# Performance work log

Hardware: AMD Instinct MI355X
Metric: run time of the kernel (lower is better)

The kernel has to match this reference:

```python
import jax, jax.numpy as jnp
import numpy as np

N_NODES = 10000
N_EDGES = 320000
IN_DIM = 512
HID = 64
H0 = 8
OUT = 64
H1 = 1
NEG_SLOPE = 0.2


def gat_layer(h, src, dst, W, attn_l, attn_r, n_nodes, activation=None):
    # h: (N, F_in); W: (F_in, H*D); attn_l/attn_r: (H, D)
    H, D = attn_l.shape
    feat = (h @ W).reshape(n_nodes, H, D)            # (N, H, D)
    el = jnp.einsum('nhd,hd->nh', feat, attn_l)      # (N, H)
    er = jnp.einsum('nhd,hd->nh', feat, attn_r)      # (N, H)
    e = jax.nn.leaky_relu(el[src] + er[dst], NEG_SLOPE)  # (E, H)
    # edge softmax over incoming edges of each destination node
    m = jax.ops.segment_max(e, dst, num_segments=n_nodes)   # (N, H), -inf for isolated
    m = jnp.where(jnp.isfinite(m), m, 0.0)
    ex = jnp.exp(e - m[dst])                         # (E, H)
    s = jax.ops.segment_sum(ex, dst, num_segments=n_nodes)  # (N, H)
    alpha = ex / s[dst]                              # (E, H)
    # weighted aggregation: out[dst] += alpha * feat[src]
    out = jax.ops.segment_sum(alpha[:, :, None] * feat[src], dst,
                              num_segments=n_nodes)  # (N, H, D)
    if activation is not None:
        out = activation(out)
    return out


def setup_inputs() -> dict:
    key = jax.random.key(0)
    ks = jax.random.split(key, 9)
    h = jax.random.normal(ks[0], (N_NODES, IN_DIM), dtype=jnp.float32)
    src = jax.random.randint(ks[1], (N_EDGES,), 0, N_NODES, dtype=jnp.int32)
    dst = jax.random.randint(ks[2], (N_EDGES,), 0, N_NODES, dtype=jnp.int32)
    W1 = jax.random.normal(ks[3], (IN_DIM, H0 * HID), dtype=jnp.float32) / np.sqrt(IN_DIM)
    attn_l1 = jax.random.normal(ks[4], (H0, HID), dtype=jnp.float32) / np.sqrt(HID)
    attn_r1 = jax.random.normal(ks[5], (H0, HID), dtype=jnp.float32) / np.sqrt(HID)
    W2 = jax.random.normal(ks[6], (H0 * HID, H1 * OUT), dtype=jnp.float32) / np.sqrt(H0 * HID)
    attn_l2 = jax.random.normal(ks[7], (H1, OUT), dtype=jnp.float32) / np.sqrt(OUT)
    attn_r2 = jax.random.normal(ks[8], (H1, OUT), dtype=jnp.float32) / np.sqrt(OUT)
    return {"h": h, "src": src, "dst": dst, "W1": W1, "attn_l1": attn_l1,
            "attn_r1": attn_r1, "W2": W2, "attn_l2": attn_l2, "attn_r2": attn_r2}


def reference(h, src, dst, W1, attn_l1, attn_r1, W2, attn_l2, attn_r2):
    # layer 1: elu activation, concat heads (flatten)
    x = gat_layer(h, src, dst, W1, attn_l1, attn_r1, N_NODES, activation=jax.nn.elu)
    x = x.reshape(N_NODES, H0 * HID)
    # layer 2: no activation, mean over heads
    x = gat_layer(x, src, dst, W2, attn_l2, attn_r2, N_NODES, activation=None)
    return x.mean(axis=1)  # (N, OUT)
```

## Files before the change

kernel.cpp:

```cpp
#include <hip/hip_runtime.h>
#include <hip/hip_bf16.h>
#include <math.h>

typedef unsigned int u32;
typedef unsigned short ushort;

constexpr int N_NODES = 10000;
constexpr int N_EDGES = 320000;
constexpr float NEG_SLOPE = 0.2f;

typedef __attribute__((ext_vector_type(8))) _Float16 half8;
typedef __attribute__((ext_vector_type(4))) float f32x4;
typedef __attribute__((ext_vector_type(16))) float f32x16;

__device__ __forceinline__ float lrelu(float x) { return x > 0.f ? x : NEG_SLOPE * x; }
__device__ __forceinline__ float elu(float x)   { return x > 0.f ? x : (expf(x) - 1.f); }

__device__ __forceinline__ ushort f2h(float x) {
    _Float16 h = (_Float16)x;
    return __builtin_bit_cast(ushort, h);
}
__device__ __forceinline__ float h2f(ushort u) {
    return (float)__builtin_bit_cast(_Float16, u);
}

__device__ __forceinline__ void gload16(const void* g, void* l) {
    __builtin_amdgcn_global_load_lds(
        (__attribute__((address_space(1))) void*)g,
        (__attribute__((address_space(3))) void*)l, 16, 0, 0);
}

constexpr int NCHUNK = 64;
constexpr int EPC    = N_EDGES / NCHUNK;
constexpr int NB_T1    = 64;
constexpr int NB_T2    = 8;
constexpr int NB_WLR2  = 2;
constexpr int NB_PRE   = NCHUNK + NB_T1 + NB_T2 + NB_WLR2;
constexpr int NB_SPLIT = (N_NODES * 512 / 4) / 256;

__global__ __launch_bounds__(256) void prep1_kernel(
                             const float4* __restrict__ h4,
                             ushort* __restrict__ xh,
                             const int* __restrict__ dst, int* __restrict__ ccnt,
                             int* __restrict__ rank,
                             const float* __restrict__ W1, ushort* __restrict__ w1t,
                             const float* __restrict__ W2, ushort* __restrict__ w2t,
                             const float* __restrict__ al2, const float* __restrict__ ar2,
                             float* __restrict__ wl2, float* __restrict__ wr2,
                             int* __restrict__ done2) {
    __shared__ __align__(16) int shbuf[N_NODES];
    const int b = blockIdx.x;
    if (b < NCHUNK) {
        for (int i = threadIdx.x; i < N_NODES; i += 256) shbuf[i] = 0;
        __syncthreads();
        const int e0 = b * EPC;
#pragma unroll 4
        for (int i = threadIdx.x; i < EPC; i += 256) {
            const int e = e0 + i;
            rank[e] = atomicAdd(&shbuf[dst[e]], 1);
        }
        __syncthreads();
        for (int i = threadIdx.x; i < N_NODES; i += 256)
            ccnt[b * N_NODES + i] = shbuf[i];
    } else if (b < NCHUNK + NB_T1 + NB_T2) {
        float* smem = (float*)shbuf;
        const int t0 = b - NCHUNK;
        const bool isW1 = t0 < NB_T1;
        const float* W = isW1 ? W1 : W2;
        ushort* wt = isW1 ? w1t : w2t;
        const int N  = isW1 ? 512 : 64;
        const int t  = isW1 ? t0 : (t0 - NB_T1);
        const int ti = isW1 ? (t & 7) : t;
        const int tj = isW1 ? (t >> 3) : 0;
        const int c  = threadIdx.x & 63;
        const int r0 = threadIdx.x >> 6;
#pragma unroll
        for (int p = 0; p < 16; p++) {
            const int r = p * 4 + r0;
            smem[r * 65 + c] = W[(size_t)(ti * 64 + r) * N + tj * 64 + c];
        }
        __syncthreads();
#pragma unroll
        for (int p = 0; p < 16; p++) {
            const int rr = p * 4 + r0;
            wt[(size_t)(tj * 64 + rr) * 512 + ti * 64 + c] = f2h(smem[c * 65 + rr]);
        }
    } else if (b < NB_PRE) {
        const int k = (b - NCHUNK - NB_T1 - NB_T2) * 256 + threadIdx.x;
        if (k == 0) done2[0] = 0;
        float sl = 0.f, sr = 0.f;
#pragma unroll 8
        for (int d = 0; d < 64; d++) {
            const float w = W2[(size_t)k * 64 + d];
            sl += w * al2[d];
            sr += w * ar2[d];
        }
        wl2[k] = sl;
        wr2[k] = sr;
    } else {
        const int i = (b - NB_PRE) * 256 + threadIdx.x;
        const float4 v = h4[i];
        *(ushort4*)&xh[i * 4] = make_ushort4(f2h(v.x), f2h(v.y), f2h(v.z), f2h(v.w));
    }
}

constexpr int NB_CSCAN = (N_NODES + 255) / 256;

__global__ __launch_bounds__(256) void scan_kernel(int* __restrict__ ccnt,
                                                   int* __restrict__ counts,
                                                   int* __restrict__ offs,
                                                   int* __restrict__ done2) {
    __shared__ int s_last;
    __shared__ int wsum[4];
    const int tid = threadIdx.x;
    const int n = blockIdx.x * 256 + tid;
    if (n < N_NODES) {
        int v[NCHUNK];
#pragma unroll
        for (int c = 0; c < NCHUNK; c++) v[c] = ccnt[c * N_NODES + n];
        int run = 0;
#pragma unroll
        for (int c = 0; c < NCHUNK; c++) {
            const int t = v[c];
            ccnt[c * N_NODES + n] = run;
            run += t;
        }
        counts[n] = run;
    }
    __threadfence();
    __syncthreads();
    if (tid == 0)
        s_last = (atomicAdd(done2, 1) == NB_CSCAN - 1) ? 1 : 0;
    __syncthreads();
    if (!s_last) return;
    __threadfence();

    const int lane = tid & 63, wave = tid >> 6;
    const int base = tid * 40;
    int v[40];
    int s = 0;
#pragma unroll
    for (int i = 0; i < 40; i++) {
        const int idx = base + i;
        v[i] = (idx < N_NODES)
            ? __hip_atomic_load(&counts[idx], __ATOMIC_RELAXED,
                                __HIP_MEMORY_SCOPE_AGENT)
            : 0;
        s += v[i];
    }
    int ps = s;
#pragma unroll
    for (int o = 1; o < 64; o <<= 1) {
        const int t = __shfl_up(ps, o);
        if (lane >= o) ps += t;
    }
    if (lane == 63) wsum[wave] = ps;
    __syncthreads();
    if (tid < 4) {
        int t = wsum[tid];
#pragma unroll
        for (int o = 1; o < 4; o <<= 1) {
            const int u = __shfl_up(t, o);
            if (tid >= o) t += u;
        }
        wsum[tid] = t;
    }
    __syncthreads();
    const int wbase = (wave > 0) ? wsum[wave - 1] : 0;
    int run = wbase + ps - s;
#pragma unroll
    for (int i = 0; i < 40; i++) {
        if (base + i < N_NODES) offs[base + i + 1] = run + v[i];
        run += v[i];
    }
    if (tid == 0) offs[0] = 0;
}

constexpr int NB_GEMM1 = ((N_NODES + 63) / 64) * 4;
constexpr int NB_SCAT  = (N_EDGES + 255) / 256;

__global__ __launch_bounds__(256) void gemm1_scatter_kernel(
    const ushort* __restrict__ A, const ushort* __restrict__ B,
    ushort* __restrict__ Cout, int M,
    const float* __restrict__ attn_l, const float* __restrict__ attn_r,
    float* __restrict__ elp, float* __restrict__ erp,
    const int* __restrict__ src, const int* __restrict__ dst,
    const int* __restrict__ rank, const int* __restrict__ offs,
    const int* __restrict__ ccnt, int* __restrict__ srcs) {
    constexpr int BM = 64, BN = 128, BK = 64, K = 512, N = 512;

    if ((int)blockIdx.x >= NB_GEMM1) {
        const int i = ((int)blockIdx.x - NB_GEMM1) * 256 + threadIdx.x;
        if (i < N_EDGES) {
            const int c = i / EPC;
            const int d = dst[i];
            srcs[offs[d] + ccnt[c * N_NODES + d] + rank[i]] = src[i];
        }
        return;
    }

    __shared__ __align__(16) ushort sA[2][BM * BK];
    __shared__ __align__(16) ushort sB[2][BN * BK];

    const int tid = threadIdx.x;
    const int wave = tid >> 6, lane = tid & 63;
    const int m0 = ((int)blockIdx.x >> 2) * BM, n0 = ((int)blockIdx.x & 3) * BN;
    const int wm = wave >> 1, wn = wave & 1;
    const int l31 = lane & 31, lh = lane >> 5;

    size_t abyte[2]; int afb[2];
#pragma unroll
    for (int p = 0; p < 2; p++) {
        const int fb = tid * 16 + p * 4096;
        const int r = fb >> 7, s = (fb >> 4) & 7;
        int ar = m0 + r; if (ar > M - 1) ar = M - 1;
        abyte[p] = (size_t)ar * (K * 2) + (size_t)((s ^ (r & 7)) << 4);
        afb[p] = fb;
    }
    size_t bbyte[4]; int bfb[4];
#pragma unroll
    for (int p = 0; p < 4; p++) {
        const int fb = tid * 16 + p * 4096;
        const int r = fb >> 7, s = (fb >> 4) & 7;
        bbyte[p] = (size_t)(n0 + r) * (K * 2) + (size_t)((s ^ (r & 7)) << 4);
        bfb[p] = fb;
    }

    f32x16 acc[2] = {};

    const int rA = wm * 32 + l31;
    const u32 aoff = rA * 128, axr = rA & 7;
    u32 boff[2], bxr[2];
#pragma unroll
    for (int ni = 0; ni < 2; ni++) {
        const int rB = wn * 64 + ni * 32 + l31;
        boff[ni] = rB * 128; bxr[ni] = rB & 7;
    }

#pragma unroll
    for (int p = 0; p < 2; p++) gload16((const char*)A + abyte[p], (char*)&sA[0][0] + afb[p]);
#pragma unroll
    for (int p = 0; p < 4; p++) gload16((const char*)B + bbyte[p], (char*)&sB[0][0] + bfb[p]);
    __syncthreads();

    int cur = 0;
    for (int k0 = 0; k0 < K; k0 += BK) {
        if (k0 + BK < K) {
            const size_t kb = (size_t)(k0 + BK) * 2;
#pragma unroll
            for (int p = 0; p < 2; p++)
                gload16((const char*)A + abyte[p] + kb, (char*)&sA[cur ^ 1][0] + afb[p]);
#pragma unroll
            for (int p = 0; p < 4; p++)
                gload16((const char*)B + bbyte[p] + kb, (char*)&sB[cur ^ 1][0] + bfb[p]);
        }
        const char* pA = (const char*)&sA[cur][0];
        const char* pB = (const char*)&sB[cur][0];
#pragma unroll
        for (int ks = 0; ks < 4; ks++) {
            const u32 sl = ks * 2 + lh;
            const half8 ah = *(const half8*)(pA + aoff + ((sl ^ axr) << 4));
#pragma unroll
            for (int ni = 0; ni < 2; ni++) {
                const half8 bh = *(const half8*)(pB + boff[ni] + ((sl ^ bxr[ni]) << 4));
                acc[ni] = __builtin_amdgcn_mfma_f32_32x32x16_f16(ah, bh, acc[ni], 0, 0, 0);
            }
        }
        __syncthreads();
        cur ^= 1;
    }

#pragma unroll
    for (int reg = 0; reg < 16; reg++) {
        const int grow = m0 + wm * 32 + (reg & 3) + 8 * (reg >> 2) + 4 * lh;
        if (grow < M) {
#pragma unroll
            for (int ni = 0; ni < 2; ni++) {
                const int gcol = n0 + wn * 64 + ni * 32 + l31;
                Cout[(size_t)grow * N + gcol] = f2h(acc[ni][reg]);
            }
        }
    }

    const int head = (n0 + wn * 64) >> 6;
    float alv[2], arv[2];
#pragma unroll
    for (int ni = 0; ni < 2; ni++) {
        alv[ni] = attn_l[head * 64 + ni * 32 + l31];
        arv[ni] = attn_r[head * 64 + ni * 32 + l31];
    }
#pragma unroll
    for (int reg = 0; reg < 16; reg++) {
        float pl = acc[0][reg] * alv[0] + acc[1][reg] * alv[1];
        float pr = acc[0][reg] * arv[0] + acc[1][reg] * arv[1];
#pragma unroll
        for (int o = 1; o < 32; o <<= 1) {
            pl += __shfl_xor(pl, o);
            pr += __shfl_xor(pr, o);
        }
        const int grow = m0 + wm * 32 + (reg & 3) + 8 * (reg >> 2) + 4 * lh;
        if (l31 == 0 && grow < M) {
            elp[grow * 8 + head] = pl;
            erp[grow * 8 + head] = pr;
        }
    }
}

__global__ __launch_bounds__(256) void gemm2_kernel(
    const ushort* __restrict__ A, const ushort* __restrict__ B,
    ushort* __restrict__ Cout, int M) {
    constexpr int BM = 32, BN = 64, BK = 64, K = 512, N = 64;

    __shared__ __align__(16) ushort sA[2][BM * BK];
    __shared__ __align__(16) ushort sB[2][BN * BK];

    const int tid = threadIdx.x;
    const int wave = tid >> 6, lane = tid & 63;
    const int m0 = blockIdx.x * BM;
    const int wm = wave >> 1, wn = wave & 1;
    const int quad = lane >> 4, l15 = lane & 15;

    const int fa = tid * 16;
    const int ra = fa >> 7, sa_ = (fa >> 4) & 7;
    int arow = m0 + ra; if (arow > M - 1) arow = M - 1;
    const size_t abyte = (size_t)arow * (K * 2) + (size_t)((sa_ ^ (ra & 7)) << 4);

    size_t bbyte[2]; int bfb[2];
#pragma unroll
    for (int p = 0; p < 2; p++) {
        const int fb = tid * 16 + p * 4096;
        const int r = fb >> 7, s = (fb >> 4) & 7;
        bbyte[p] = (size_t)r * (K * 2) + (size_t)((s ^ (r & 7)) << 4);
        bfb[p] = fb;
    }

    f32x4 acc[2] = {};
    const int rA = wm * 16 + l15;
    const u32 aoff = rA * 128, axr = rA & 7;
    u32 boff[2], bxr[2];
#pragma unroll
    for (int ni = 0; ni < 2; ni++) {
        const int rB = wn * 32 + ni * 16 + l15;
        boff[ni] = rB * 128; bxr[ni] = rB & 7;
    }

    gload16((const char*)A + abyte, (char*)&sA[0][0] + fa);
#pragma unroll
    for (int p = 0; p < 2; p++) gload16((const char*)B + bbyte[p], (char*)&sB[0][0] + bfb[p]);
    __syncthreads();

    int cur = 0;
    for (int k0 = 0; k0 < K; k0 += BK) {
        if (k0 + BK < K) {
            const size_t kb = (size_t)(k0 + BK) * 2;
            gload16((const char*)A + abyte + kb, (char*)&sA[cur ^ 1][0] + fa);
#pragma unroll
            for (int p = 0; p < 2; p++)
                gload16((const char*)B + bbyte[p] + kb, (char*)&sB[cur ^ 1][0] + bfb[p]);
        }
        const char* pA = (const char*)&sA[cur][0];
        const char* pB = (const char*)&sB[cur][0];
#pragma unroll
        for (int ks = 0; ks < 2; ks++) {
            const u32 sl = ks * 4 + quad;
            const half8 ah = *(const half8*)(pA + aoff + ((sl ^ axr) << 4));
#pragma unroll
            for (int ni = 0; ni < 2; ni++) {
                const half8 bh = *(const half8*)(pB + boff[ni] + ((sl ^ bxr[ni]) << 4));
                acc[ni] = __builtin_amdgcn_mfma_f32_16x16x32_f16(ah, bh, acc[ni], 0, 0, 0);
            }
        }
        __syncthreads();
        cur ^= 1;
    }

#pragma unroll
    for (int r = 0; r < 4; r++) {
        const int grow = m0 + wm * 16 + quad * 4 + r;
        if (grow < M) {
#pragma unroll
            for (int ni = 0; ni < 2; ni++) {
                const int gcol = wn * 32 + ni * 16 + l15;
                Cout[(size_t)grow * N + gcol] = f2h(acc[ni][r]);
            }
        }
    }
}

__global__ __launch_bounds__(256) void agg1_kernel(
    const ushort* __restrict__ feat, const float* __restrict__ el,
    const float* __restrict__ er, const int* __restrict__ offs,
    const int* __restrict__ srcs, ushort* __restrict__ xh,
    const float* __restrict__ wl2, const float* __restrict__ wr2,
    float* __restrict__ el2, float* __restrict__ er2) {
    const int tid = threadIdx.x;
    const int wave = tid >> 6, lane = tid & 63;
    const int node = blockIdx.x * 4 + wave;
    const int start = offs[node];
    const int deg = offs[node + 1] - start;
    const int d0 = lane * 8;
    const int myh = lane >> 3;

    if (deg == 0) {
        const ushort4 z = make_ushort4(0, 0, 0, 0);
        *(ushort4*)&xh[(size_t)node * 512 + d0] = z;
        *(ushort4*)&xh[(size_t)node * 512 + d0 + 4] = z;
        if (lane == 0) { el2[node] = 0.f; er2[node] = 0.f; }
        return;
    }

    const float4 ea = *(const float4*)&er[node * 8];
    const float4 eb = *(const float4*)&er[node * 8 + 4];
    const float er_my = (myh & 4) ? ((myh & 2) ? ((myh & 1) ? eb.w : eb.z)
                                              : ((myh & 1) ? eb.y : eb.x))
                                  : ((myh & 2) ? ((myh & 1) ? ea.w : ea.z)
                                              : ((myh & 1) ? ea.y : ea.x));

    float acc[8];
#pragma unroll
    for (int i = 0; i < 8; i++) acc[i] = 0.f;
    float ws = 0.f;

    for (int base = 0; base < deg; base += 64) {
        const int has = min(64, deg - base);
        const int s = srcs[start + base + min(lane, has - 1)];
        int j = 0;
        for (; j + 8 <= has; j += 8) {
            int sq[8];
#pragma unroll
            for (int q = 0; q < 8; q++) sq[q] = __shfl(s, j + q);
            float eq[8];
#pragma unroll
            for (int q = 0; q < 8; q++) eq[q] = el[sq[q] * 8 + myh];
            half8 uq[8];
#pragma unroll
            for (int q = 0; q < 8; q++)
                uq[q] = *(const half8*)&feat[(size_t)sq[q] * 512 + d0];
            float wq[8];
#pragma unroll
            for (int q = 0; q < 8; q++) wq[q] = __expf(lrelu(eq[q] + er_my));
#pragma unroll
            for (int q = 0; q < 8; q++) {
#pragma unroll
                for (int i = 0; i < 8; i++)
                    acc[i] += wq[q] * (float)uq[q][i];
                ws += wq[q];
            }
        }
        for (; j < has; j++) {
            const int sj = __shfl(s, j);
            const float w = __expf(lrelu(el[sj * 8 + myh] + er_my));
            const half8 u = *(const half8*)&feat[(size_t)sj * 512 + d0];
#pragma unroll
            for (int i = 0; i < 8; i++)
                acc[i] += w * (float)u[i];
            ws += w;
        }
    }

    const float inv = 1.f / ws;
    float o[8];
#pragma unroll
    for (int i = 0; i < 8; i++) o[i] = elu(acc[i] * inv);

    const float4 wla = *(const float4*)&wl2[d0];
    const float4 wlb = *(const float4*)&wl2[d0 + 4];
    const float4 wra = *(const float4*)&wr2[d0];
    const float4 wrb = *(const float4*)&wr2[d0 + 4];
    float pl = o[0] * wla.x + o[1] * wla.y + o[2] * wla.z + o[3] * wla.w
             + o[4] * wlb.x + o[5] * wlb.y + o[6] * wlb.z + o[7] * wlb.w;
    float pr = o[0] * wra.x + o[1] * wra.y + o[2] * wra.z + o[3] * wra.w
             + o[4] * wrb.x + o[5] * wrb.y + o[6] * wrb.z + o[7] * wrb.w;
#pragma unroll
    for (int off = 32; off > 0; off >>= 1) {
        pl += __shfl_xor(pl, off);
        pr += __shfl_xor(pr, off);
    }
    if (lane == 0) { el2[node] = pl; er2[node] = pr; }

    ushort hh[8];
#pragma unroll
    for (int i = 0; i < 8; i++) hh[i] = f2h(o[i]);
    *(ushort4*)&xh[(size_t)node * 512 + d0]     = make_ushort4(hh[0], hh[1], hh[2], hh[3]);
    *(ushort4*)&xh[(size_t)node * 512 + d0 + 4] = make_ushort4(hh[4], hh[5], hh[6], hh[7]);
}

__global__ __launch_bounds__(256) void agg2_kernel(
    const ushort* __restrict__ feat, const float* __restrict__ el,
    const float* __restrict__ er, const int* __restrict__ offs,
    const int* __restrict__ srcs, float* __restrict__ out) {
    const int tid = threadIdx.x;
    const int wave = tid >> 6, lane = tid & 63;
    const int node = blockIdx.x * 4 + wave;
    const int start = offs[node];
    const int deg = offs[node + 1] - start;
    if (deg == 0) { out[(size_t)node * 64 + lane] = 0.f; return; }
    const float ern = er[node];

    float acc = 0.f, ws = 0.f;
    for (int base = 0; base < deg; base += 64) {
        const int has = min(64, deg - base);
        const int s = srcs[start + base + min(lane, has - 1)];
        const float w = __expf(lrelu(el[s] + ern));
        int j = 0;
        for (; j + 8 <= has; j += 8) {
            float aq[8]; int sq[8];
#pragma unroll
            for (int q = 0; q < 8; q++) { aq[q] = __shfl(w, j + q); sq[q] = __shfl(s, j + q); }
            ushort fq[8];
#pragma unroll
            for (int q = 0; q < 8; q++) fq[q] = feat[(size_t)sq[q] * 64 + lane];
#pragma unroll
            for (int q = 0; q < 8; q++) { acc += aq[q] * h2f(fq[q]); ws += aq[q]; }
        }
        for (; j < has; j++) {
            const float a = __shfl(w, j);
            const int sj = __shfl(s, j);
            acc += a * h2f(feat[(size_t)sj * 64 + lane]);
            ws += a;
        }
    }
    out[(size_t)node * 64 + lane] = acc / ws;
}

extern "C" void kernel_launch(void* const* d_in, const int* in_sizes, int n_in,
                              void* d_out, int out_size, void* d_ws, size_t ws_size,
                              hipStream_t stream) {
    const float* h   = (const float*)d_in[0];
    const int*   src = (const int*)d_in[1];
    const int*   dst = (const int*)d_in[2];
    const float* W1  = (const float*)d_in[3];
    const float* al1 = (const float*)d_in[4];
    const float* ar1 = (const float*)d_in[5];
    const float* W2  = (const float*)d_in[6];
    const float* al2 = (const float*)d_in[7];
    const float* ar2 = (const float*)d_in[8];
    float* out = (float*)d_out;

    char* p = (char*)d_ws;
    ushort* feat1 = (ushort*)p; p += (size_t)N_NODES * 512 * 2;
    ushort* feat2 = (ushort*)p; p += (size_t)N_NODES * 64 * 2;
    float* el1   = (float*)p;  p += (size_t)N_NODES * 8 * 4;
    float* er1   = (float*)p;  p += (size_t)N_NODES * 8 * 4;
    float* el2   = (float*)p;  p += (size_t)N_NODES * 4;
    float* er2   = (float*)p;  p += (size_t)N_NODES * 4;
    ushort* xh   = (ushort*)p; p += (size_t)N_NODES * 512 * 2;
    ushort* w1t  = (ushort*)p; p += (size_t)512 * 512 * 2;
    ushort* w2t  = (ushort*)p; p += (size_t)64 * 512 * 2;
    float* wl2   = (float*)p;  p += (size_t)512 * 4;
    float* wr2   = (float*)p;  p += (size_t)512 * 4;
    int* counts  = (int*)p;    p += (size_t)N_NODES * 4;
    int* done2   = (int*)p;    p += 16;
    int* ccnt    = (int*)p;    p += (size_t)NCHUNK * N_NODES * 4;
    int* offs    = (int*)p;    p += (size_t)10004 * 4;
    int* rank    = (int*)p;    p += (size_t)N_EDGES * 4;
    int* srcs    = (int*)p;    p += (size_t)N_EDGES * 4;

    prep1_kernel<<<NB_PRE + NB_SPLIT, 256, 0, stream>>>(
        (const float4*)h, xh, dst, ccnt, rank,
        W1, w1t, W2, w2t, al2, ar2, wl2, wr2, done2);

    scan_kernel<<<NB_CSCAN, 256, 0, stream>>>(ccnt, counts, offs, done2);

    gemm1_scatter_kernel<<<NB_GEMM1 + NB_SCAT, 256, 0, stream>>>(
        xh, w1t, feat1, N_NODES, al1, ar1, el1, er1,
        src, dst, rank, offs, ccnt, srcs);

    agg1_kernel<<<N_NODES / 4, 256, 0, stream>>>(
        feat1, el1, er1, offs, srcs, xh, wl2, wr2, el2, er2);

    gemm2_kernel<<<(N_NODES + 31) / 32, 256, 0, stream>>>(
        xh, w2t, feat2, N_NODES);

    agg2_kernel<<<N_NODES / 4, 256, 0, stream>>>(feat2, el2, er2, offs, srcs, out);
}
```

Before: 183.9 us.

## Precompute per-edge attention weights and split layer-1 aggregation across four column slices

Adds a per-edge kernel that computes the exp(leaky_relu(el+er)) weights for all 8 heads into a CSR-ordered buffer, using a new sorted-destination array written during the scatter. The layer-1 aggregation now runs four blocks per node group, each wave covering a 128-column slice with 2 halves per lane, which raises parallelism and reads the precomputed weights instead of gathering el per edge. Per-slice partial attention dot products are reduced in extra blocks appended to gemm2. The cost is an extra kernel launch, a 10 MB weight buffer written and then read, and four times as many srcs and weight loads per node.

```diff
diff --git a/kernel.cpp b/kernel.cpp
--- a/kernel.cpp
+++ b/kernel.cpp
@@ -186,7 +186,8 @@
     float* __restrict__ elp, float* __restrict__ erp,
     const int* __restrict__ src, const int* __restrict__ dst,
     const int* __restrict__ rank, const int* __restrict__ offs,
-    const int* __restrict__ ccnt, int* __restrict__ srcs) {
+    const int* __restrict__ ccnt, int* __restrict__ srcs,
+    int* __restrict__ dsts_s) {
     constexpr int BM = 64, BN = 128, BK = 64, K = 512, N = 512;
 
     if ((int)blockIdx.x >= NB_GEMM1) {
@@ -194,7 +195,9 @@
         if (i < N_EDGES) {
             const int c = i / EPC;
             const int d = dst[i];
-            srcs[offs[d] + ccnt[c * N_NODES + d] + rank[i]] = src[i];
+            const int slot = offs[d] + ccnt[c * N_NODES + d] + rank[i];
+            srcs[slot] = src[i];
+            dsts_s[slot] = d;
         }
         return;
     }
@@ -306,10 +309,126 @@
     }
 }
 
+constexpr int NB_WEXP = (N_EDGES + 255) / 256;
+
+__global__ __launch_bounds__(256) void wexp_kernel(
+    const int* __restrict__ srcs, const int* __restrict__ dsts_s,
+    const float* __restrict__ el, const float* __restrict__ er,
+    float* __restrict__ wexp) {
+    const int i = blockIdx.x * 256 + threadIdx.x;
+    if (i >= N_EDGES) return;
+    const int s = srcs[i], d = dsts_s[i];
+    const float4 ea = *(const float4*)&el[s * 8];
+    const float4 eb = *(const float4*)&el[s * 8 + 4];
+    const float4 ra = *(const float4*)&er[d * 8];
+    const float4 rb = *(const float4*)&er[d * 8 + 4];
+    float4 w0, w1;
+    w0.x = __expf(lrelu(ea.x + ra.x));
+    w0.y = __expf(lrelu(ea.y + ra.y));
+    w0.z = __expf(lrelu(ea.z + ra.z));
+    w0.w = __expf(lrelu(ea.w + ra.w));
+    w1.x = __expf(lrelu(eb.x + rb.x));
+    w1.y = __expf(lrelu(eb.y + rb.y));
+    w1.z = __expf(lrelu(eb.z + rb.z));
+    w1.w = __expf(lrelu(eb.w + rb.w));
+    *(float4*)&wexp[(size_t)i * 8]     = w0;
+    *(float4*)&wexp[(size_t)i * 8 + 4] = w1;
+}
+
+constexpr int NB_AGG1 = (N_NODES / 4) * 4;
+
+__global__ __launch_bounds__(256) void agg1_kernel(
+    const ushort* __restrict__ feat, const float* __restrict__ wexp,
+    const int* __restrict__ offs, const int* __restrict__ srcs,
+    ushort* __restrict__ xh,
+    const float* __restrict__ wl2, const float* __restrict__ wr2,
+    float* __restrict__ plp, float* __restrict__ prp) {
+    const int tid = threadIdx.x;
+    const int wave = tid >> 6, lane = tid & 63;
+    const int pair = blockIdx.x & 3;
+    const int node = (blockIdx.x >> 2) * 4 + wave;
+    const int start = offs[node];
+    const int deg = offs[node + 1] - start;
+    const int d0 = pair * 128 + lane * 2;
+
+    if (deg == 0) {
+        *(ushort2*)&xh[(size_t)node * 512 + d0] = make_ushort2(0, 0);
+        if (lane == 0) { plp[node * 4 + pair] = 0.f; prp[node * 4 + pair] = 0.f; }
+        return;
+    }
+
+    const int wsel = pair * 2 + (lane >> 5);
+    float acc0 = 0.f, acc1 = 0.f, ws = 0.f;
+
+    for (int base = 0; base < deg; base += 64) {
+        const int has = min(64, deg - base);
+        const int s = __builtin_nontemporal_load(&srcs[start + base + min(lane, has - 1)]);
+        int j = 0;
+        for (; j + 8 <= has; j += 8) {
+            int sq[8];
+#pragma unroll
+            for (int q = 0; q < 8; q++) sq[q] = __shfl(s, j + q);
+            float wq[8];
+#pragma unroll
+            for (int q = 0; q < 8; q++)
+                wq[q] = __builtin_nontemporal_load(
+                    &wexp[(size_t)(start + base + j + q) * 8 + wsel]);
+            u32 fq[8];
+#pragma unroll
+            for (int q = 0; q < 8; q++)
+                fq[q] = *(const u32*)&feat[(size_t)sq[q] * 512 + d0];
+#pragma unroll
+            for (int q = 0; q < 8; q++) {
+                const float w = wq[q];
+                acc0 += w * h2f((ushort)(fq[q] & 0xffff));
+                acc1 += w * h2f((ushort)(fq[q] >> 16));
+                ws += w;
+            }
+        }
+        for (; j < has; j++) {
+            const int sj = __shfl(s, j);
+            const float w = __builtin_nontemporal_load(
+                &wexp[(size_t)(start + base + j) * 8 + wsel]);
+            const u32 f = *(const u32*)&feat[(size_t)sj * 512 + d0];
+            acc0 += w * h2f((ushort)(f & 0xffff));
+            acc1 += w * h2f((ushort)(f >> 16));
+            ws += w;
+        }
+    }
+
+    const float inv = 1.f / ws;
+    const float o0 = elu(acc0 * inv);
+    const float o1 = elu(acc1 * inv);
+    *(ushort2*)&xh[(size_t)node * 512 + d0] = make_ushort2(f2h(o0), f2h(o1));
+
+    float pl = o0 * wl2[d0] + o1 * wl2[d0 + 1];
+    float pr = o0 * wr2[d0] + o1 * wr2[d0 + 1];
+#pragma unroll
+    for (int off = 32; off > 0; off >>= 1) {
+        pl += __shfl_xor(pl, off);
+        pr += __shfl_xor(pr, off);
+    }
+    if (lane == 0) { plp[node * 4 + pair] = pl; prp[node * 4 + pair] = pr; }
+}
+
+constexpr int NB_G2  = (N_NODES + 31) / 32;
+constexpr int NB_SUM = (N_NODES + 255) / 256;
+
 __global__ __launch_bounds__(256) void gemm2_kernel(
     const ushort* __restrict__ A, const ushort* __restrict__ B,
-    ushort* __restrict__ Cout, int M) {
+    ushort* __restrict__ Cout, int M,
+    const float* __restrict__ plp, const float* __restrict__ prp,
+    float* __restrict__ el2, float* __restrict__ er2) {
     constexpr int BM = 32, BN = 64, BK = 64, K = 512, N = 64;
+
+    if ((int)blockIdx.x >= NB_G2) {
+        const int n = ((int)blockIdx.x - NB_G2) * 256 + threadIdx.x;
+        if (n < N_NODES) {
+            el2[n] = plp[n * 4] + plp[n * 4 + 1] + plp[n * 4 + 2] + plp[n * 4 + 3];
+            er2[n] = prp[n * 4] + prp[n * 4 + 1] + prp[n * 4 + 2] + prp[n * 4 + 3];
+        }
+        return;
+    }
 
     __shared__ __align__(16) ushort sA[2][BM * BK];
     __shared__ __align__(16) ushort sB[2][BN * BK];
@@ -385,104 +504,6 @@
             }
         }
     }
-}
-
-__global__ __launch_bounds__(256) void agg1_kernel(
-    const ushort* __restrict__ feat, const float* __restrict__ el,
-    const float* __restrict__ er, const int* __restrict__ offs,
-    const int* __restrict__ srcs, ushort* __restrict__ xh,
-    const float* __restrict__ wl2, const float* __restrict__ wr2,
-    float* __restrict__ el2, float* __restrict__ er2) {
-    const int tid = threadIdx.x;
-    const int wave = tid >> 6, lane = tid & 63;
-    const int node = blockIdx.x * 4 + wave;
-    const int start = offs[node];
-    const int deg = offs[node + 1] - start;
-    const int d0 = lane * 8;
-    const int myh = lane >> 3;
-
-    if (deg == 0) {
-        const ushort4 z = make_ushort4(0, 0, 0, 0);
-        *(ushort4*)&xh[(size_t)node * 512 + d0] = z;
-        *(ushort4*)&xh[(size_t)node * 512 + d0 + 4] = z;
-        if (lane == 0) { el2[node] = 0.f; er2[node] = 0.f; }
-        return;
-    }
-
-    const float4 ea = *(const float4*)&er[node * 8];
-    const float4 eb = *(const float4*)&er[node * 8 + 4];
-    const float er_my = (myh & 4) ? ((myh & 2) ? ((myh & 1) ? eb.w : eb.z)
-                                              : ((myh & 1) ? eb.y : eb.x))
-                                  : ((myh & 2) ? ((myh & 1) ? ea.w : ea.z)
-                                              : ((myh & 1) ? ea.y : ea.x));
-
-    float acc[8];
-#pragma unroll
-    for (int i = 0; i < 8; i++) acc[i] = 0.f;
-    float ws = 0.f;
-
-    for (int base = 0; base < deg; base += 64) {
-        const int has = min(64, deg - base);
-        const int s = srcs[start + base + min(lane, has - 1)];
-        int j = 0;
-        for (; j + 8 <= has; j += 8) {
-            int sq[8];
-#pragma unroll
-            for (int q = 0; q < 8; q++) sq[q] = __shfl(s, j + q);
-            float eq[8];
-#pragma unroll
-            for (int q = 0; q < 8; q++) eq[q] = el[sq[q] * 8 + myh];
-            half8 uq[8];
-#pragma unroll
-            for (int q = 0; q < 8; q++)
-                uq[q] = *(const half8*)&feat[(size_t)sq[q] * 512 + d0];
-            float wq[8];
-#pragma unroll
-            for (int q = 0; q < 8; q++) wq[q] = __expf(lrelu(eq[q] + er_my));
-#pragma unroll
-            for (int q = 0; q < 8; q++) {
-#pragma unroll
-                for (int i = 0; i < 8; i++)
-                    acc[i] += wq[q] * (float)uq[q][i];
-                ws += wq[q];
-            }
-        }
-        for (; j < has; j++) {
-            const int sj = __shfl(s, j);
-            const float w = __expf(lrelu(el[sj * 8 + myh] + er_my));
-            const half8 u = *(const half8*)&feat[(size_t)sj * 512 + d0];
-#pragma unroll
-            for (int i = 0; i < 8; i++)
-                acc[i] += w * (float)u[i];
-            ws += w;
-        }
-    }
-
-    const float inv = 1.f / ws;
-    float o[8];
-#pragma unroll
-    for (int i = 0; i < 8; i++) o[i] = elu(acc[i] * inv);
-
-    const float4 wla = *(const float4*)&wl2[d0];
-    const float4 wlb = *(const float4*)&wl2[d0 + 4];
-    const float4 wra = *(const float4*)&wr2[d0];
-    const float4 wrb = *(const float4*)&wr2[d0 + 4];
-    float pl = o[0] * wla.x + o[1] * wla.y + o[2] * wla.z + o[3] * wla.w
-             + o[4] * wlb.x + o[5] * wlb.y + o[6] * wlb.z + o[7] * wlb.w;
-    float pr = o[0] * wra.x + o[1] * wra.y + o[2] * wra.z + o[3] * wra.w
-             + o[4] * wrb.x + o[5] * wrb.y + o[6] * wrb.z + o[7] * wrb.w;
-#pragma unroll
-    for (int off = 32; off > 0; off >>= 1) {
-        pl += __shfl_xor(pl, off);
-        pr += __shfl_xor(pr, off);
-    }
-    if (lane == 0) { el2[node] = pl; er2[node] = pr; }
-
-    ushort hh[8];
-#pragma unroll
-    for (int i = 0; i < 8; i++) hh[i] = f2h(o[i]);
-    *(ushort4*)&xh[(size_t)node * 512 + d0]     = make_ushort4(hh[0], hh[1], hh[2], hh[3]);
-    *(ushort4*)&xh[(size_t)node * 512 + d0 + 4] = make_ushort4(hh[4], hh[5], hh[6], hh[7]);
 }
 
 __global__ __launch_bounds__(256) void agg2_kernel(
@@ -555,6 +576,10 @@
     int* offs    = (int*)p;    p += (size_t)10004 * 4;
     int* rank    = (int*)p;    p += (size_t)N_EDGES * 4;
     int* srcs    = (int*)p;    p += (size_t)N_EDGES * 4;
+    int* dsts_s  = (int*)p;    p += (size_t)N_EDGES * 4;
+    float* wexp  = (float*)p;  p += (size_t)N_EDGES * 8 * 4;
+    float* plp   = (float*)p;  p += (size_t)N_NODES * 4 * 4;
+    float* prp   = (float*)p;  p += (size_t)N_NODES * 4 * 4;
 
     prep1_kernel<<<NB_PRE + NB_SPLIT, 256, 0, stream>>>(
         (const float4*)h, xh, dst, ccnt, rank,
@@ -564,13 +589,15 @@
 
     gemm1_scatter_kernel<<<NB_GEMM1 + NB_SCAT, 256, 0, stream>>>(
         xh, w1t, feat1, N_NODES, al1, ar1, el1, er1,
-        src, dst, rank, offs, ccnt, srcs);
-
-    agg1_kernel<<<N_NODES / 4, 256, 0, stream>>>(
-        feat1, el1, er1, offs, srcs, xh, wl2, wr2, el2, er2);
-
-    gemm2_kernel<<<(N_NODES + 31) / 32, 256, 0, stream>>>(
-        xh, w2t, feat2, N_NODES);
+        src, dst, rank, offs, ccnt, srcs, dsts_s);
+
+    wexp_kernel<<<NB_WEXP, 256, 0, stream>>>(srcs, dsts_s, el1, er1, wexp);
+
+    agg1_kernel<<<NB_AGG1, 256, 0, stream>>>(
+        feat1, wexp, offs, srcs, xh, wl2, wr2, plp, prp);
+
+    gemm2_kernel<<<NB_G2 + NB_SUM, 256, 0, stream>>>(
+        xh, w2t, feat2, N_NODES, plp, prp, el2, er2);
 
     agg2_kernel<<<N_NODES / 4, 256, 0, stream>>>(feat2, el2, er2, offs, srcs, out);
 }
```

Result: slower. 211.4 us (+15.0%).

## Precompute per-edge layer-1 attention exp weights in a separate kernel

Applied to the files above, without the earlier changes.

Adds a wexp kernel that computes exp(leaky_relu(el[src]+er[dst])) for all 8 heads of each CSR-sorted edge and stores it. The scatter step now also writes the sorted destination index. agg1 then reads these weights contiguously instead of gathering el per edge and running exp inline. This takes the scattered el gather and the exp math out of the aggregation loop, at the cost of an extra kernel launch and about 10 MB of extra global writes and reads. The gemm2 kernel is only moved in the file.

```diff
diff --git a/kernel.cpp b/kernel.cpp
--- a/kernel.cpp
+++ b/kernel.cpp
@@ -186,7 +186,8 @@
     float* __restrict__ elp, float* __restrict__ erp,
     const int* __restrict__ src, const int* __restrict__ dst,
     const int* __restrict__ rank, const int* __restrict__ offs,
-    const int* __restrict__ ccnt, int* __restrict__ srcs) {
+    const int* __restrict__ ccnt, int* __restrict__ srcs,
+    int* __restrict__ dsts_s) {
     constexpr int BM = 64, BN = 128, BK = 64, K = 512, N = 512;
 
     if ((int)blockIdx.x >= NB_GEMM1) {
@@ -194,7 +195,9 @@
         if (i < N_EDGES) {
             const int c = i / EPC;
             const int d = dst[i];
-            srcs[offs[d] + ccnt[c * N_NODES + d] + rank[i]] = src[i];
+            const int slot = offs[d] + ccnt[c * N_NODES + d] + rank[i];
+            srcs[slot] = src[i];
+            dsts_s[slot] = d;
         }
         return;
     }
@@ -306,91 +309,36 @@
     }
 }
 
-__global__ __launch_bounds__(256) void gemm2_kernel(
-    const ushort* __restrict__ A, const ushort* __restrict__ B,
-    ushort* __restrict__ Cout, int M) {
-    constexpr int BM = 32, BN = 64, BK = 64, K = 512, N = 64;
-
-    __shared__ __align__(16) ushort sA[2][BM * BK];
-    __shared__ __align__(16) ushort sB[2][BN * BK];
-
-    const int tid = threadIdx.x;
-    const int wave = tid >> 6, lane = tid & 63;
-    const int m0 = blockIdx.x * BM;
-    const int wm = wave >> 1, wn = wave & 1;
-    const int quad = lane >> 4, l15 = lane & 15;
-
-    const int fa = tid * 16;
-    const int ra = fa >> 7, sa_ = (fa >> 4) & 7;
-    int arow = m0 + ra; if (arow > M - 1) arow = M - 1;
-    const size_t abyte = (size_t)arow * (K * 2) + (size_t)((sa_ ^ (ra & 7)) << 4);
-
-    size_t bbyte[2]; int bfb[2];
-#pragma unroll
-    for (int p = 0; p < 2; p++) {
-        const int fb = tid * 16 + p * 4096;
-        const int r = fb >> 7, s = (fb >> 4) & 7;
-        bbyte[p] = (size_t)r * (K * 2) + (size_t)((s ^ (r & 7)) << 4);
-        bfb[p] = fb;
-    }
-
-    f32x4 acc[2] = {};
-    const int rA = wm * 16 + l15;
-    const u32 aoff = rA * 128, axr = rA & 7;
-    u32 boff[2], bxr[2];
-#pragma unroll
-    for (int ni = 0; ni < 2; ni++) {
-        const int rB = wn * 32 + ni * 16 + l15;
-        boff[ni] = rB * 128; bxr[ni] = rB & 7;
-    }
-
-    gload16((const char*)A + abyte, (char*)&sA[0][0] + fa);
-#pragma unroll
-    for (int p = 0; p < 2; p++) gload16((const char*)B + bbyte[p], (char*)&sB[0][0] + bfb[p]);
-    __syncthreads();
-
-    int cur = 0;
-    for (int k0 = 0; k0 < K; k0 += BK) {
-        if (k0 + BK < K) {
-            const size_t kb = (size_t)(k0 + BK) * 2;
-            gload16((const char*)A + abyte + kb, (char*)&sA[cur ^ 1][0] + fa);
-#pragma unroll
-            for (int p = 0; p < 2; p++)
-                gload16((const char*)B + bbyte[p] + kb, (char*)&sB[cur ^ 1][0] + bfb[p]);
-        }
-        const char* pA = (const char*)&sA[cur][0];
-        const char* pB = (const char*)&sB[cur][0];
-#pragma unroll
-        for (int ks = 0; ks < 2; ks++) {
-            const u32 sl = ks * 4 + quad;
-            const half8 ah = *(const half8*)(pA + aoff + ((sl ^ axr) << 4));
-#pragma unroll
-            for (int ni = 0; ni < 2; ni++) {
-                const half8 bh = *(const half8*)(pB + boff[ni] + ((sl ^ bxr[ni]) << 4));
-                acc[ni] = __builtin_amdgcn_mfma_f32_16x16x32_f16(ah, bh, acc[ni], 0, 0, 0);
-            }
-        }
-        __syncthreads();
-        cur ^= 1;
-    }
-
-#pragma unroll
-    for (int r = 0; r < 4; r++) {
-        const int grow = m0 + wm * 16 + quad * 4 + r;
-        if (grow < M) {
-#pragma unroll
-            for (int ni = 0; ni < 2; ni++) {
-                const int gcol = wn * 32 + ni * 16 + l15;
-                Cout[(size_t)grow * N + gcol] = f2h(acc[ni][r]);
-            }
-        }
-    }
+constexpr int NB_WEXP = (N_EDGES + 255) / 256;
+
+__global__ __launch_bounds__(256) void wexp_kernel(
+    const int* __restrict__ srcs, const int* __restrict__ dsts_s,
+    const float* __restrict__ el, const float* __restrict__ er,
+    float* __restrict__ wexp) {
+    const int i = blockIdx.x * 256 + threadIdx.x;
+    if (i >= N_EDGES) return;
+    const int s = srcs[i], d = dsts_s[i];
+    const float4 ea = *(const float4*)&el[s * 8];
+    const float4 eb = *(const float4*)&el[s * 8 + 4];
+    const float4 ra = *(const float4*)&er[d * 8];
+    const float4 rb = *(const float4*)&er[d * 8 + 4];
+    float4 w0, w1;
+    w0.x = __expf(lrelu(ea.x + ra.x));
+    w0.y = __expf(lrelu(ea.y + ra.y));
+    w0.z = __expf(lrelu(ea.z + ra.z));
+    w0.w = __expf(lrelu(ea.w + ra.w));
+    w1.x = __expf(lrelu(eb.x + rb.x));
+    w1.y = __expf(lrelu(eb.y + rb.y));
+    w1.z = __expf(lrelu(eb.z + rb.z));
+    w1.w = __expf(lrelu(eb.w + rb.w));
+    *(float4*)&wexp[(size_t)i * 8]     = w0;
+    *(float4*)&wexp[(size_t)i * 8 + 4] = w1;
 }
 
 __global__ __launch_bounds__(256) void agg1_kernel(
-    const ushort* __restrict__ feat, const float* __restrict__ el,
-    const float* __restrict__ er, const int* __restrict__ offs,
-    const int* __restrict__ srcs, ushort* __restrict__ xh,
+    const ushort* __restrict__ feat, const float* __restrict__ wexp,
+    const int* __restrict__ offs, const int* __restrict__ srcs,
+    ushort* __restrict__ xh,
     const float* __restrict__ wl2, const float* __restrict__ wr2,
     float* __restrict__ el2, float* __restrict__ er2) {
     const int tid = threadIdx.x;
@@ -409,13 +357,6 @@
         return;
     }
 
-    const float4 ea = *(const float4*)&er[node * 8];
-    const float4 eb = *(const float4*)&er[node * 8 + 4];
-    const float er_my = (myh & 4) ? ((myh & 2) ? ((myh & 1) ? eb.w : eb.z)
-                                              : ((myh & 1) ? eb.y : eb.x))
-                                  : ((myh & 2) ? ((myh & 1) ? ea.w : ea.z)
-                                              : ((myh & 1) ? ea.y : ea.x));
-
     float acc[8];
 #pragma unroll
     for (int i = 0; i < 8; i++) acc[i] = 0.f;
@@ -429,16 +370,14 @@
             int sq[8];
 #pragma unroll
             for (int q = 0; q < 8; q++) sq[q] = __shfl(s, j + q);
-            float eq[8];
-#pragma unroll
-            for (int q = 0; q < 8; q++) eq[q] = el[sq[q] * 8 + myh];
+            float wq[8];
+#pragma unroll
+            for (int q = 0; q < 8; q++)
+                wq[q] = wexp[(size_t)(start + base + j + q) * 8 + myh];
             half8 uq[8];
 #pragma unroll
             for (int q = 0; q < 8; q++)
                 uq[q] = *(const half8*)&feat[(size_t)sq[q] * 512 + d0];
-            float wq[8];
-#pragma unroll
-            for (int q = 0; q < 8; q++) wq[q] = __expf(lrelu(eq[q] + er_my));
 #pragma unroll
             for (int q = 0; q < 8; q++) {
 #pragma unroll
@@ -449,7 +388,7 @@
         }
         for (; j < has; j++) {
             const int sj = __shfl(s, j);
-            const float w = __expf(lrelu(el[sj * 8 + myh] + er_my));
+            const float w = wexp[(size_t)(start + base + j) * 8 + myh];
             const half8 u = *(const half8*)&feat[(size_t)sj * 512 + d0];
 #pragma unroll
             for (int i = 0; i < 8; i++)
@@ -483,6 +422,87 @@
     for (int i = 0; i < 8; i++) hh[i] = f2h(o[i]);
     *(ushort4*)&xh[(size_t)node * 512 + d0]     = make_ushort4(hh[0], hh[1], hh[2], hh[3]);
     *(ushort4*)&xh[(size_t)node * 512 + d0 + 4] = make_ushort4(hh[4], hh[5], hh[6], hh[7]);
+}
+
+__global__ __launch_bounds__(256) void gemm2_kernel(
+    const ushort* __restrict__ A, const ushort* __restrict__ B,
+    ushort* __restrict__ Cout, int M) {
+    constexpr int BM = 32, BN = 64, BK = 64, K = 512, N = 64;
+
+    __shared__ __align__(16) ushort sA[2][BM * BK];
+    __shared__ __align__(16) ushort sB[2][BN * BK];
+
+    const int tid = threadIdx.x;
+    const int wave = tid >> 6, lane = tid & 63;
+    const int m0 = blockIdx.x * BM;
+    const int wm = wave >> 1, wn = wave & 1;
+    const int quad = lane >> 4, l15 = lane & 15;
+
+    const int fa = tid * 16;
+    const int ra = fa >> 7, sa_ = (fa >> 4) & 7;
+    int arow = m0 + ra; if (arow > M - 1) arow = M - 1;
+    const size_t abyte = (size_t)arow * (K * 2) + (size_t)((sa_ ^ (ra & 7)) << 4);
+
+    size_t bbyte[2]; int bfb[2];
+#pragma unroll
+    for (int p = 0; p < 2; p++) {
+        const int fb = tid * 16 + p * 4096;
+        const int r = fb >> 7, s = (fb >> 4) & 7;
+        bbyte[p] = (size_t)r * (K * 2) + (size_t)((s ^ (r & 7)) << 4);
+        bfb[p] = fb;
+    }
+
+    f32x4 acc[2] = {};
+    const int rA = wm * 16 + l15;
+    const u32 aoff = rA * 128, axr = rA & 7;
+    u32 boff[2], bxr[2];
+#pragma unroll
+    for (int ni = 0; ni < 2; ni++) {
+        const int rB = wn * 32 + ni * 16 + l15;
+        boff[ni] = rB * 128; bxr[ni] = rB & 7;
+    }
+
+    gload16((const char*)A + abyte, (char*)&sA[0][0] + fa);
+#pragma unroll
+    for (int p = 0; p < 2; p++) gload16((const char*)B + bbyte[p], (char*)&sB[0][0] + bfb[p]);
+    __syncthreads();
+
+    int cur = 0;
+    for (int k0 = 0; k0 < K; k0 += BK) {
+        if (k0 + BK < K) {
+            const size_t kb = (size_t)(k0 + BK) * 2;
+            gload16((const char*)A + abyte + kb, (char*)&sA[cur ^ 1][0] + fa);
+#pragma unroll
+            for (int p = 0; p < 2; p++)
+                gload16((const char*)B + bbyte[p] + kb, (char*)&sB[cur ^ 1][0] + bfb[p]);
+        }
+        const char* pA = (const char*)&sA[cur][0];
+        const char* pB = (const char*)&sB[cur][0];
+#pragma unroll
+        for (int ks = 0; ks < 2; ks++) {
+            const u32 sl = ks * 4 + quad;
+            const half8 ah = *(const half8*)(pA + aoff + ((sl ^ axr) << 4));
+#pragma unroll
+            for (int ni = 0; ni < 2; ni++) {
+                const half8 bh = *(const half8*)(pB + boff[ni] + ((sl ^ bxr[ni]) << 4));
+                acc[ni] = __builtin_amdgcn_mfma_f32_16x16x32_f16(ah, bh, acc[ni], 0, 0, 0);
+            }
+        }
+        __syncthreads();
+        cur ^= 1;
+    }
+
+#pragma unroll
+    for (int r = 0; r < 4; r++) {
+        const int grow = m0 + wm * 16 + quad * 4 + r;
+        if (grow < M) {
+#pragma unroll
+            for (int ni = 0; ni < 2; ni++) {
+                const int gcol = wn * 32 + ni * 16 + l15;
+                Cout[(size_t)grow * N + gcol] = f2h(acc[ni][r]);
+            }
+        }
+    }
 }
 
 __global__ __launch_bounds__(256) void agg2_kernel(
@@ -555,6 +575,8 @@
     int* offs    = (int*)p;    p += (size_t)10004 * 4;
     int* rank    = (int*)p;    p += (size_t)N_EDGES * 4;
     int* srcs    = (int*)p;    p += (size_t)N_EDGES * 4;
+    int* dsts_s  = (int*)p;    p += (size_t)N_EDGES * 4;
+    float* wexp  = (float*)p;  p += (size_t)N_EDGES * 8 * 4;
 
     prep1_kernel<<<NB_PRE + NB_SPLIT, 256, 0, stream>>>(
         (const float4*)h, xh, dst, ccnt, rank,
@@ -564,10 +586,12 @@
 
     gemm1_scatter_kernel<<<NB_GEMM1 + NB_SCAT, 256, 0, stream>>>(
         xh, w1t, feat1, N_NODES, al1, ar1, el1, er1,
-        src, dst, rank, offs, ccnt, srcs);
+        src, dst, rank, offs, ccnt, srcs, dsts_s);
+
+    wexp_kernel<<<NB_WEXP, 256, 0, stream>>>(srcs, dsts_s, el1, er1, wexp);
 
     agg1_kernel<<<N_NODES / 4, 256, 0, stream>>>(
-        feat1, el1, er1, offs, srcs, xh, wl2, wr2, el2, er2);
+        feat1, wexp, offs, srcs, xh, wl2, wr2, el2, er2);
 
     gemm2_kernel<<<(N_NODES + 31) / 32, 256, 0, stream>>>(
         xh, w2t, feat2, N_NODES);
```

Result: slower. 196.3 us (+6.8%).
